# Kernel tuning notes

Measured on AMD Instinct MI355X. Metric: run time of the kernel, lower is better.

## Reference

```python
import jax, jax.numpy as jnp
import numpy as np

B, T = 512, 256
DX, DZ, DH, DDZ, DDX = 1024, 256, 512, 256, 256


def setup_inputs() -> dict:
    key = jax.random.key(0)
    ks = jax.random.split(key, 16)
    s = 0.05
    return {
        "eps": jax.random.normal(ks[0], (B, T, DZ), jnp.float32),
        # stoch_trans dz: h -> relu -> (loc, softplus scale)
        "dz_W1": jax.random.normal(ks[1], (DDZ, DH), jnp.float32) * s,
        "dz_b1": jnp.zeros((DDZ,), jnp.float32),
        "dz_Wloc": jax.random.normal(ks[2], (DZ, DDZ), jnp.float32) * s,
        "dz_bloc": jnp.zeros((DZ,), jnp.float32),
        "dz_Wscale": jax.random.normal(ks[3], (DZ, DDZ), jnp.float32) * s,
        "dz_bscale": jnp.zeros((DZ,), jnp.float32),
        # GRU cell (PyTorch layout: gates [r, z, n] stacked)
        "gru_Wih": jax.random.normal(ks[4], (3 * DH, DZ), jnp.float32) * s,
        "gru_Whh": jax.random.normal(ks[5], (3 * DH, DH), jnp.float32) * s,
        "gru_bih": jnp.zeros((3 * DH,), jnp.float32),
        "gru_bhh": jnp.zeros((3 * DH,), jnp.float32),
        # emitter dx: h -> relu -> sigmoid probs
        "dx_W1": jax.random.normal(ks[6], (DDX, DH), jnp.float32) * s,
        "dx_b1": jnp.zeros((DDX,), jnp.float32),
        "dx_W2": jax.random.normal(ks[7], (DX, DDX), jnp.float32) * s,
        "dx_b2": jnp.zeros((DX,), jnp.float32),
        "h0": jnp.zeros((DH,), jnp.float32),
    }


def reference(eps, dz_W1, dz_b1, dz_Wloc, dz_bloc, dz_Wscale, dz_bscale,
              gru_Wih, gru_Whh, gru_bih, gru_bhh,
              dx_W1, dx_b1, dx_W2, dx_b2, h0):
    batch = eps.shape[0]
    h_init = jnp.broadcast_to(h0[None, :], (batch, h0.shape[0]))

    def step(h, eps_t):
        # stochastic transition: z_loc, z_scale from h_{t-1}
        hid = jax.nn.relu(h @ dz_W1.T + dz_b1)
        z_loc = hid @ dz_Wloc.T + dz_bloc
        z_scale = jax.nn.softplus(hid @ dz_Wscale.T + dz_bscale)
        z_t = z_loc + z_scale * eps_t  # reparameterized Normal sample
        # GRU cell (torch equations)
        gi = z_t @ gru_Wih.T + gru_bih
        gh = h @ gru_Whh.T + gru_bhh
        i_r, i_z, i_n = jnp.split(gi, 3, axis=-1)
        h_r, h_z, h_n = jnp.split(gh, 3, axis=-1)
        r = jax.nn.sigmoid(i_r + h_r)
        u = jax.nn.sigmoid(i_z + h_z)
        n = jnp.tanh(i_n + r * h_n)
        h_new = (1.0 - u) * n + u * h
        # emitter: Bernoulli probs
        hid2 = jax.nn.relu(h_new @ dx_W1.T + dx_b1)
        x_ps = jax.nn.sigmoid(hid2 @ dx_W2.T + dx_b2)
        return h_new, x_ps

    eps_tb = jnp.swapaxes(eps, 0, 1)  # [T, B, DZ]
    _, x_ps = jax.lax.scan(step, h_init, eps_tb)
    return jnp.swapaxes(x_ps, 0, 1)  # [B, T, DX]
```

## Files before the change

kernel.cpp:

```cpp
#include <hip/hip_runtime.h>
#include <hip/hip_bf16.h>

#define DEV __device__ __forceinline__

typedef __bf16 bf16x8 __attribute__((ext_vector_type(8)));
typedef float  f32x4  __attribute__((ext_vector_type(4)));

constexpr int BB  = 512;
constexpr int TT  = 256;
constexpr int DX  = 1024;
constexpr int DZ  = 256;
constexpr int DH  = 512;

DEV f32x4 mfma16(bf16x8 a, bf16x8 b, f32x4 c) {
    return __builtin_amdgcn_mfma_f32_16x16x32_bf16(a, b, c, 0, 0, 0);
}
DEV float sigf(float x) { return 1.0f / (1.0f + __expf(-x)); }
DEV float tanhf_(float x) {
    float e = __expf(-2.0f * fabsf(x));
    float r = (1.0f - e) / (1.0f + e);
    return copysignf(r, x);
}
DEV float softplusf(float x) {
    float m = fmaxf(x, 0.0f);
    return m + __logf(__expf(x - m) + __expf(-m));
}

DEV void st16_wt(void* p, bf16x8 v) {
    asm volatile("global_store_dwordx4 %0, %1, off sc0 sc1" :: "v"(p), "v"(v) : "memory");
}
DEV void st_flag(unsigned* p, unsigned v) {
    asm volatile("global_store_dword %0, %1, off sc0 sc1" :: "v"(p), "v"(v) : "memory");
}
DEV unsigned ld_flag(const unsigned* p) {
    unsigned v;
    asm volatile("global_load_dword %0, %1, off sc0 sc1\n\ts_waitcnt vmcnt(0)"
                 : "=v"(v) : "v"(p) : "memory");
    return v;
}
#define CC_LOAD(dst, p) \
    asm volatile("global_load_dwordx4 %0, %1, off sc0 sc1" : "=v"(dst) : "v"(p))
#define VMCNT0 do { \
    asm volatile("s_waitcnt vmcnt(0)" ::: "memory"); \
    __builtin_amdgcn_sched_barrier(0); } while (0)
#define LGKM0 do { \
    asm volatile("s_waitcnt lgkmcnt(0)" ::: "memory"); \
    __builtin_amdgcn_sched_barrier(0); } while (0)

DEV void wave_wait(const unsigned* base, int nslots, int wv, unsigned tgt) {
    const int lane = threadIdx.x & 63;
    const unsigned* p = base + (((lane & (nslots - 1)) * 4 + wv) * 32);
    while (true) {
        unsigned v = ld_flag(p);
        if (__all((int)(v >= tgt))) break;
    }
}

struct CvtArgs {
    const float* src[7];
    __bf16* dst[7];
    int n[7];
};
__global__ void cvt_weights(CvtArgs a, const float* h0, __bf16* h0buf) {
    int idx = blockIdx.x * blockDim.x + threadIdx.x;
    int stride = gridDim.x * blockDim.x;
    for (int s = 0; s < 7; ++s) {
        const float* sp = a.src[s];
        __bf16* dp = a.dst[s];
        int n = a.n[s];
        for (int i = idx; i < n; i += stride) dp[i] = (__bf16)sp[i];
    }
    for (int i = idx; i < 512 * 512; i += stride) h0buf[i] = (__bf16)h0[i & 511];
}

__global__ __launch_bounds__(256, 1) void phase1c(
    const float* __restrict__ eps,
    const float* __restrict__ b1,  const float* __restrict__ bloc,
    const float* __restrict__ bscale, const float* __restrict__ bih,
    const float* __restrict__ bhh,
    const __bf16* __restrict__ wW1,   const __bf16* __restrict__ wWloc,
    const __bf16* __restrict__ wWscale, const __bf16* __restrict__ wWih,
    const __bf16* __restrict__ wWhh,
    const __bf16* __restrict__ h0buf,
    unsigned* __restrict__ flags,
    char* __restrict__ outb)
{
    __shared__ __bf16 lds[75776];

    const int tid  = threadIdx.x;
    const int w    = tid >> 6;
    const int lane = tid & 63;
    const int r16  = lane & 15;
    const int g4   = lane >> 4;
    const int g    = blockIdx.x & 7;
    const int r    = blockIdx.x >> 3;
    unsigned* gfl   = flags + g * 4096;
    unsigned* flagA = gfl;
    unsigned* flagB = gfl + 2048;
    unsigned* flagC = gfl + 3072;
    const int rowW  = g * 64 + w * 16;

    auto stage = [&](const __bf16* src, __bf16* dst, int R, int C) {
        int chunks = R * C / 8;
        for (int ch = tid; ch < chunks; ch += 256) {
            int row = ch / (C / 8), cc = (ch % (C / 8)) * 8;
            bf16x8 v = *(const bf16x8*)(src + (size_t)row * C + cc);
            *(bf16x8*)(dst + ((row * C + cc) ^ ((row & 7) << 3))) = v;
        }
    };

    if (r < 8) {
        stage(wW1     + (size_t)(r * 32) * 512, lds,         32, 512);
        stage(wWloc   + (size_t)(r * 32) * 256, lds + 16384, 32, 256);
        stage(wWscale + (size_t)(r * 32) * 256, lds + 24576, 32, 256);
        __bf16* wb = lds + 32768 + w * 512;
        const int zc0 = r * 32;
        float bb1[2], bbl[2], bbs[2];
        #pragma unroll
        for (int tt = 0; tt < 2; ++tt) {
            int c = zc0 + tt * 16 + r16;
            bb1[tt] = b1[c]; bbl[tt] = bloc[c]; bbs[tt] = bscale[c];
        }
        __syncthreads();

        for (int t = 0; t < TT; ++t) {
            float ev[2][4];
            #pragma unroll
            for (int tt = 0; tt < 2; ++tt)
                #pragma unroll
                for (int i = 0; i < 4; ++i) {
                    int row = rowW + 4 * g4 + i;
                    ev[tt][i] = __builtin_nontemporal_load(
                        eps + ((size_t)row * TT + t) * DZ + zc0 + tt * 16 + r16);
                }
            if (t) wave_wait(flagA, 16, w, t);
            const char* hp = (t == 0)
                ? (const char*)(h0buf + (size_t)(rowW + r16) * 512) + g4 * 16
                : outb + ((size_t)(rowW + r16) * TT + (t - 1)) * 4096 + 2048 + g4 * 16;
            bf16x8 hv[16];
            #pragma unroll
            for (int kk = 0; kk < 16; ++kk) CC_LOAD(hv[kk], hp + kk * 64);
            VMCNT0;
            f32x4 acc0 = {0,0,0,0}, acc1 = {0,0,0,0};
            #pragma unroll
            for (int kk = 0; kk < 16; ++kk) {
                int l0 = r16, l1 = 16 + r16;
                acc0 = mfma16(hv[kk], *(const bf16x8*)(lds + ((l0 * 512 + kk * 32 + g4 * 8) ^ ((l0 & 7) << 3))), acc0);
                acc1 = mfma16(hv[kk], *(const bf16x8*)(lds + ((l1 * 512 + kk * 32 + g4 * 8) ^ ((l1 & 7) << 3))), acc1);
            }
            #pragma unroll
            for (int tt = 0; tt < 2; ++tt) {
                f32x4 ac = tt ? acc1 : acc0;
                #pragma unroll
                for (int i = 0; i < 4; ++i)
                    wb[(4 * g4 + i) * 32 + tt * 16 + r16] = (__bf16)fmaxf(ac[i] + bb1[tt], 0.0f);
            }
            LGKM0;
            {
                int rl = lane >> 2, ch = lane & 3;
                bf16x8 v = *(const bf16x8*)(wb + rl * 32 + ch * 8);
                st16_wt(outb + ((size_t)(rowW + rl) * TT + t) * 4096 + 3072 + (zc0 + ch * 8) * 2, v);
            }
            VMCNT0;
            if (lane == 0) st_flag(flagB + (r * 4 + w) * 32, t + 1);
            wave_wait(flagB, 8, w, t + 1);
            const char* qp = outb + ((size_t)(rowW + r16) * TT + t) * 4096 + 3072 + g4 * 16;
            bf16x8 qv[8];
            #pragma unroll
            for (int kk = 0; kk < 8; ++kk) CC_LOAD(qv[kk], qp + kk * 64);
            VMCNT0;
            f32x4 aL0 = {0,0,0,0}, aL1 = {0,0,0,0}, aS0 = {0,0,0,0}, aS1 = {0,0,0,0};
            #pragma unroll
            for (int kk = 0; kk < 8; ++kk) {
                int l0 = r16, l1 = 16 + r16;
                int s0 = (l0 * 256 + kk * 32 + g4 * 8) ^ ((l0 & 7) << 3);
                int s1 = (l1 * 256 + kk * 32 + g4 * 8) ^ ((l1 & 7) << 3);
                aL0 = mfma16(qv[kk], *(const bf16x8*)(lds + 16384 + s0), aL0);
                aL1 = mfma16(qv[kk], *(const bf16x8*)(lds + 16384 + s1), aL1);
                aS0 = mfma16(qv[kk], *(const bf16x8*)(lds + 24576 + s0), aS0);
                aS1 = mfma16(qv[kk], *(const bf16x8*)(lds + 24576 + s1), aS1);
            }
            #pragma unroll
            for (int tt = 0; tt < 2; ++tt) {
                f32x4 L = tt ? aL1 : aL0, S = tt ? aS1 : aS0;
                #pragma unroll
                for (int i = 0; i < 4; ++i) {
                    float z = (L[i] + bbl[tt]) + softplusf(S[i] + bbs[tt]) * ev[tt][i];
                    wb[(4 * g4 + i) * 32 + tt * 16 + r16] = (__bf16)z;
                }
            }
            LGKM0;
            {
                int rl = lane >> 2, ch = lane & 3;
                bf16x8 v = *(const bf16x8*)(wb + rl * 32 + ch * 8);
                st16_wt(outb + ((size_t)(rowW + rl) * TT + t) * 4096 + 3584 + (zc0 + ch * 8) * 2, v);
            }
            VMCNT0;
            if (lane == 0) st_flag(flagC + (r * 4 + w) * 32, t + 1);
        }
    } else {
        const int c0 = (r - 8) * 32;
        for (int gg = 0; gg < 3; ++gg) {
            stage(wWhh + (size_t)(512 * gg + c0) * 512, lds + gg * 16384, 32, 512);
            stage(wWih + (size_t)(512 * gg + c0) * 256, lds + 49152 + gg * 8192, 32, 256);
        }
        __bf16* wb = lds + 73728 + w * 512;
        float bI[3][2], bH[3][2];
        #pragma unroll
        for (int gg = 0; gg < 3; ++gg)
            #pragma unroll
            for (int tt = 0; tt < 2; ++tt) {
                int col = 512 * gg + c0 + tt * 16 + r16;
                bI[gg][tt] = bih[col];
                bH[gg][tt] = bhh[col];
            }
        float hreg[2][4];
        #pragma unroll
        for (int tt = 0; tt < 2; ++tt) {
            float v = (float)h0buf[c0 + tt * 16 + r16];
            #pragma unroll
            for (int i = 0; i < 4; ++i) hreg[tt][i] = v;
        }
        __syncthreads();

        for (int t = 0; t < TT; ++t) {
            if (t) wave_wait(flagA, 16, w, t);
            const char* hp = (t == 0)
                ? (const char*)(h0buf + (size_t)(rowW + r16) * 512) + g4 * 16
                : outb + ((size_t)(rowW + r16) * TT + (t - 1)) * 4096 + 2048 + g4 * 16;
            bf16x8 hv[16];
            #pragma unroll
            for (int kk = 0; kk < 16; ++kk) CC_LOAD(hv[kk], hp + kk * 64);
            VMCNT0;
            f32x4 gh[6];
            #pragma unroll
            for (int j = 0; j < 6; ++j) gh[j] = (f32x4){0,0,0,0};
            #pragma unroll
            for (int kk = 0; kk < 16; ++kk) {
                #pragma unroll
                for (int j = 0; j < 6; ++j) {
                    int gg = j >> 1, lr = (j & 1) * 16 + r16;
                    gh[j] = mfma16(hv[kk], *(const bf16x8*)(lds + gg * 16384 +
                              ((lr * 512 + kk * 32 + g4 * 8) ^ ((lr & 7) << 3))), gh[j]);
                }
            }
            wave_wait(flagC, 8, w, t + 1);
            const char* zp = outb + ((size_t)(rowW + r16) * TT + t) * 4096 + 3584 + g4 * 16;
            bf16x8 zv[8];
            #pragma unroll
            for (int kk = 0; kk < 8; ++kk) CC_LOAD(zv[kk], zp + kk * 64);
            VMCNT0;
            f32x4 gi[6];
            #pragma unroll
            for (int j = 0; j < 6; ++j) gi[j] = (f32x4){0,0,0,0};
            #pragma unroll
            for (int kk = 0; kk < 8; ++kk) {
                #pragma unroll
                for (int j = 0; j < 6; ++j) {
                    int gg = j >> 1, lr = (j & 1) * 16 + r16;
                    gi[j] = mfma16(zv[kk], *(const bf16x8*)(lds + 49152 + gg * 8192 +
                              ((lr * 256 + kk * 32 + g4 * 8) ^ ((lr & 7) << 3))), gi[j]);
                }
            }
            #pragma unroll
            for (int tt = 0; tt < 2; ++tt) {
                #pragma unroll
                for (int i = 0; i < 4; ++i) {
                    float rr = sigf(gi[0 + tt][i] + bI[0][tt] + gh[0 + tt][i] + bH[0][tt]);
                    float uu = sigf(gi[2 + tt][i] + bI[1][tt] + gh[2 + tt][i] + bH[1][tt]);
                    float nn = tanhf_(gi[4 + tt][i] + bI[2][tt] + rr * (gh[4 + tt][i] + bH[2][tt]));
                    float hv2 = (1.0f - uu) * nn + uu * hreg[tt][i];
                    hreg[tt][i] = hv2;
                    wb[(4 * g4 + i) * 32 + tt * 16 + r16] = (__bf16)hv2;
                }
            }
            LGKM0;
            {
                int rl = lane >> 2, ch = lane & 3;
                bf16x8 v = *(const bf16x8*)(wb + rl * 32 + ch * 8);
                st16_wt(outb + ((size_t)(rowW + rl) * TT + t) * 4096 + 2048 + (c0 + ch * 8) * 2, v);
            }
            VMCNT0;
            if (lane == 0) st_flag(flagA + ((r - 8) * 4 + w) * 32, t + 1);
        }
    }
}

__global__ __launch_bounds__(256, 3) void phase2(
    const float* __restrict__ db1, const float* __restrict__ db2,
    const __bf16* __restrict__ W1, const __bf16* __restrict__ W2,
    float* __restrict__ out)
{
    __shared__ __bf16 hS  [32 * 512];
    __shared__ __bf16 hid2[32 * 256];

    const int tid  = threadIdx.x;
    const int w    = tid >> 6;
    const int lane = tid & 63;
    const int r16  = lane & 15;
    const int g4   = lane >> 4;
    const size_t row0 = (size_t)blockIdx.x * 32;

    #pragma unroll
    for (int it = 0; it < 8; ++it) {
        int chunk = it * 256 + tid;
        int row = chunk >> 6;
        int cc  = (chunk & 63) * 8;
        bf16x8 v = __builtin_nontemporal_load(
            (const bf16x8*)((const char*)out + (row0 + row) * 4096 + 2048 + cc * 2));
        *(bf16x8*)(hS + ((row * 512 + cc) ^ ((row & 7) << 3))) = v;
    }
    __syncthreads();

    {
        f32x4 acc[2][4];
        #pragma unroll
        for (int rt = 0; rt < 2; ++rt)
            #pragma unroll
            for (int ct = 0; ct < 4; ++ct) acc[rt][ct] = (f32x4){0,0,0,0};
        const __bf16* pB[4];
        #pragma unroll
        for (int ct = 0; ct < 4; ++ct)
            pB[ct] = W1 + (w * 64 + 16 * ct + r16) * 512 + g4 * 8;
        #pragma unroll
        for (int kk = 0; kk < 16; ++kk) {
            bf16x8 a[2];
            #pragma unroll
            for (int rt = 0; rt < 2; ++rt) {
                int row = rt * 16 + r16;
                a[rt] = *(const bf16x8*)(hS + ((row * 512 + kk * 32 + g4 * 8) ^ ((row & 7) << 3)));
            }
            #pragma unroll
            for (int ct = 0; ct < 4; ++ct) {
                bf16x8 b = *(const bf16x8*)(pB[ct] + kk * 32);
                acc[0][ct] = mfma16(a[0], b, acc[0][ct]);
                acc[1][ct] = mfma16(a[1], b, acc[1][ct]);
            }
        }
        #pragma unroll
        for (int ct = 0; ct < 4; ++ct) {
            int col = w * 64 + 16 * ct + r16;
            float bias = db1[col];
            #pragma unroll
            for (int rt = 0; rt < 2; ++rt)
                #pragma unroll
                for (int i = 0; i < 4; ++i) {
                    int row = rt * 16 + g4 * 4 + i;
                    hid2[(row * 256 + col) ^ ((row & 7) << 3)] =
                        (__bf16)fmaxf(acc[rt][ct][i] + bias, 0.0f);
                }
        }
    }
    __syncthreads();

    #pragma unroll
    for (int c = 0; c < 4; ++c) {
        f32x4 acc[2][4];
        #pragma unroll
        for (int rt = 0; rt < 2; ++rt)
            #pragma unroll
            for (int ct = 0; ct < 4; ++ct) acc[rt][ct] = (f32x4){0,0,0,0};
        const __bf16* pB[4];
        #pragma unroll
        for (int ct = 0; ct < 4; ++ct)
            pB[ct] = W2 + (w * 256 + c * 64 + 16 * ct + r16) * 256 + g4 * 8;
        #pragma unroll
        for (int kk = 0; kk < 8; ++kk) {
            bf16x8 a[2];
            #pragma unroll
            for (int rt = 0; rt < 2; ++rt) {
                int row = rt * 16 + r16;
                a[rt] = *(const bf16x8*)(hid2 + ((row * 256 + kk * 32 + g4 * 8) ^ ((row & 7) << 3)));
            }
            #pragma unroll
            for (int ct = 0; ct < 4; ++ct) {
                bf16x8 b = *(const bf16x8*)(pB[ct] + kk * 32);
                acc[0][ct] = mfma16(a[0], b, acc[0][ct]);
                acc[1][ct] = mfma16(a[1], b, acc[1][ct]);
            }
        }
        #pragma unroll
        for (int ct = 0; ct < 4; ++ct) {
            int col = w * 256 + c * 64 + 16 * ct + r16;
            float bias = db2[col];
            #pragma unroll
            for (int rt = 0; rt < 2; ++rt)
                #pragma unroll
                for (int i = 0; i < 4; ++i) {
                    int row = rt * 16 + g4 * 4 + i;
                    __builtin_nontemporal_store(sigf(acc[rt][ct][i] + bias),
                                                out + (row0 + row) * DX + col);
                }
        }
    }
}

extern "C" void kernel_launch(void* const* d_in, const int* in_sizes, int n_in,
                              void* d_out, int out_size, void* d_ws, size_t ws_size,
                              hipStream_t stream) {
    const float* eps       = (const float*)d_in[0];
    const float* dz_W1     = (const float*)d_in[1];
    const float* dz_b1     = (const float*)d_in[2];
    const float* dz_Wloc   = (const float*)d_in[3];
    const float* dz_bloc   = (const float*)d_in[4];
    const float* dz_Wscale = (const float*)d_in[5];
    const float* dz_bscale = (const float*)d_in[6];
    const float* gru_Wih   = (const float*)d_in[7];
    const float* gru_Whh   = (const float*)d_in[8];
    const float* gru_bih   = (const float*)d_in[9];
    const float* gru_bhh   = (const float*)d_in[10];
    const float* dx_W1     = (const float*)d_in[11];
    const float* dx_b1     = (const float*)d_in[12];
    const float* dx_W2     = (const float*)d_in[13];
    const float* dx_b2     = (const float*)d_in[14];
    const float* h0        = (const float*)d_in[15];
    float* out = (float*)d_out;
    char* ws = (char*)d_ws;

    __bf16* wW1     = (__bf16*)(ws + 0);
    __bf16* wWloc   = (__bf16*)(ws + 262144);
    __bf16* wWscale = (__bf16*)(ws + 393216);
    __bf16* wWih    = (__bf16*)(ws + 524288);
    __bf16* wWhh    = (__bf16*)(ws + 1310720);
    __bf16* wdxW1   = (__bf16*)(ws + 2883584);
    __bf16* wdxW2   = (__bf16*)(ws + 3145728);
    __bf16* h0buf   = (__bf16*)(ws + 3670016);
    unsigned* flags = (unsigned*)(ws + 4194304);

    hipMemsetAsync(flags, 0, 131072, stream);

    CvtArgs ca;
    ca.src[0] = dz_W1;     ca.dst[0] = wW1;     ca.n[0] = 256 * 512;
    ca.src[1] = dz_Wloc;   ca.dst[1] = wWloc;   ca.n[1] = 256 * 256;
    ca.src[2] = dz_Wscale; ca.dst[2] = wWscale; ca.n[2] = 256 * 256;
    ca.src[3] = gru_Wih;   ca.dst[3] = wWih;    ca.n[3] = 1536 * 256;
    ca.src[4] = gru_Whh;   ca.dst[4] = wWhh;    ca.n[4] = 1536 * 512;
    ca.src[5] = dx_W1;     ca.dst[5] = wdxW1;   ca.n[5] = 256 * 512;
    ca.src[6] = dx_W2;     ca.dst[6] = wdxW2;   ca.n[6] = 1024 * 256;

    cvt_weights<<<1024, 256, 0, stream>>>(ca, h0, h0buf);
    phase1c<<<192, 256, 0, stream>>>(eps, dz_b1, dz_bloc, dz_bscale,
                                     gru_bih, gru_bhh,
                                     wW1, wWloc, wWscale, wWih, wWhh,
                                     h0buf, flags, (char*)out);
    phase2<<<(BB * TT) / 32, 256, 0, stream>>>(dx_b1, dx_b2, wdxW1, wdxW2, out);
}
```

Measured before the change: 2.819 ms.

## Halve waves per block in recurrent kernel, each wave handles two row slabs

The persistent recurrent kernel now runs 128 threads per block instead of 256. Each wave processes two 16-row sub-slabs sequentially, and flag slots are re-indexed per (wave, sub-slab). This cuts the number of waves contending for the CU and the number of flag pollers, and lets one wave overlap its sub-slab work with the flag waits of another. The cost is that per-step latency per wave roughly doubles and the critical path through the recurrence becomes more serial.

```diff
diff --git a/kernel.cpp b/kernel.cpp
--- a/kernel.cpp
+++ b/kernel.cpp
@@ -47,9 +47,9 @@
     asm volatile("s_waitcnt lgkmcnt(0)" ::: "memory"); \
     __builtin_amdgcn_sched_barrier(0); } while (0)
 
-DEV void wave_wait(const unsigned* base, int nslots, int wv, unsigned tgt) {
+DEV void waitP(const unsigned* base, int mask, int w, int s, unsigned tgt) {
     const int lane = threadIdx.x & 63;
-    const unsigned* p = base + (((lane & (nslots - 1)) * 4 + wv) * 32);
+    const unsigned* p = base + (((lane & mask) * 2 + w) * 2 + s) * 32;
     while (true) {
         unsigned v = ld_flag(p);
         if (__all((int)(v >= tgt))) break;
@@ -73,7 +73,7 @@
     for (int i = idx; i < 512 * 512; i += stride) h0buf[i] = (__bf16)h0[i & 511];
 }
 
-__global__ __launch_bounds__(256, 1) void phase1c(
+__global__ __launch_bounds__(128, 1) void phase1c(
     const float* __restrict__ eps,
     const float* __restrict__ b1,  const float* __restrict__ bloc,
     const float* __restrict__ bscale, const float* __restrict__ bih,
@@ -98,11 +98,11 @@
     unsigned* flagA = gfl;
     unsigned* flagB = gfl + 2048;
     unsigned* flagC = gfl + 3072;
-    const int rowW  = g * 64 + w * 16;
+    const int rowBase = g * 64 + w * 32;
 
     auto stage = [&](const __bf16* src, __bf16* dst, int R, int C) {
         int chunks = R * C / 8;
-        for (int ch = tid; ch < chunks; ch += 256) {
+        for (int ch = tid; ch < chunks; ch += 128) {
             int row = ch / (C / 8), cc = (ch % (C / 8)) * 8;
             bf16x8 v = *(const bf16x8*)(src + (size_t)row * C + cc);
             *(bf16x8*)(dst + ((row * C + cc) ^ ((row & 7) << 3))) = v;
@@ -124,79 +124,89 @@
         __syncthreads();
 
         for (int t = 0; t < TT; ++t) {
-            float ev[2][4];
-            #pragma unroll
-            for (int tt = 0; tt < 2; ++tt)
-                #pragma unroll
-                for (int i = 0; i < 4; ++i) {
-                    int row = rowW + 4 * g4 + i;
-                    ev[tt][i] = __builtin_nontemporal_load(
-                        eps + ((size_t)row * TT + t) * DZ + zc0 + tt * 16 + r16);
-                }
-            if (t) wave_wait(flagA, 16, w, t);
-            const char* hp = (t == 0)
-                ? (const char*)(h0buf + (size_t)(rowW + r16) * 512) + g4 * 16
-                : outb + ((size_t)(rowW + r16) * TT + (t - 1)) * 4096 + 2048 + g4 * 16;
-            bf16x8 hv[16];
-            #pragma unroll
-            for (int kk = 0; kk < 16; ++kk) CC_LOAD(hv[kk], hp + kk * 64);
-            VMCNT0;
-            f32x4 acc0 = {0,0,0,0}, acc1 = {0,0,0,0};
-            #pragma unroll
-            for (int kk = 0; kk < 16; ++kk) {
-                int l0 = r16, l1 = 16 + r16;
-                acc0 = mfma16(hv[kk], *(const bf16x8*)(lds + ((l0 * 512 + kk * 32 + g4 * 8) ^ ((l0 & 7) << 3))), acc0);
-                acc1 = mfma16(hv[kk], *(const bf16x8*)(lds + ((l1 * 512 + kk * 32 + g4 * 8) ^ ((l1 & 7) << 3))), acc1);
-            }
-            #pragma unroll
-            for (int tt = 0; tt < 2; ++tt) {
-                f32x4 ac = tt ? acc1 : acc0;
-                #pragma unroll
-                for (int i = 0; i < 4; ++i)
-                    wb[(4 * g4 + i) * 32 + tt * 16 + r16] = (__bf16)fmaxf(ac[i] + bb1[tt], 0.0f);
-            }
-            LGKM0;
-            {
-                int rl = lane >> 2, ch = lane & 3;
-                bf16x8 v = *(const bf16x8*)(wb + rl * 32 + ch * 8);
-                st16_wt(outb + ((size_t)(rowW + rl) * TT + t) * 4096 + 3072 + (zc0 + ch * 8) * 2, v);
-            }
-            VMCNT0;
-            if (lane == 0) st_flag(flagB + (r * 4 + w) * 32, t + 1);
-            wave_wait(flagB, 8, w, t + 1);
-            const char* qp = outb + ((size_t)(rowW + r16) * TT + t) * 4096 + 3072 + g4 * 16;
-            bf16x8 qv[8];
-            #pragma unroll
-            for (int kk = 0; kk < 8; ++kk) CC_LOAD(qv[kk], qp + kk * 64);
-            VMCNT0;
-            f32x4 aL0 = {0,0,0,0}, aL1 = {0,0,0,0}, aS0 = {0,0,0,0}, aS1 = {0,0,0,0};
-            #pragma unroll
-            for (int kk = 0; kk < 8; ++kk) {
-                int l0 = r16, l1 = 16 + r16;
-                int s0 = (l0 * 256 + kk * 32 + g4 * 8) ^ ((l0 & 7) << 3);
-                int s1 = (l1 * 256 + kk * 32 + g4 * 8) ^ ((l1 & 7) << 3);
-                aL0 = mfma16(qv[kk], *(const bf16x8*)(lds + 16384 + s0), aL0);
-                aL1 = mfma16(qv[kk], *(const bf16x8*)(lds + 16384 + s1), aL1);
-                aS0 = mfma16(qv[kk], *(const bf16x8*)(lds + 24576 + s0), aS0);
-                aS1 = mfma16(qv[kk], *(const bf16x8*)(lds + 24576 + s1), aS1);
-            }
-            #pragma unroll
-            for (int tt = 0; tt < 2; ++tt) {
-                f32x4 L = tt ? aL1 : aL0, S = tt ? aS1 : aS0;
-                #pragma unroll
-                for (int i = 0; i < 4; ++i) {
-                    float z = (L[i] + bbl[tt]) + softplusf(S[i] + bbs[tt]) * ev[tt][i];
-                    wb[(4 * g4 + i) * 32 + tt * 16 + r16] = (__bf16)z;
-                }
-            }
-            LGKM0;
-            {
-                int rl = lane >> 2, ch = lane & 3;
-                bf16x8 v = *(const bf16x8*)(wb + rl * 32 + ch * 8);
-                st16_wt(outb + ((size_t)(rowW + rl) * TT + t) * 4096 + 3584 + (zc0 + ch * 8) * 2, v);
-            }
-            VMCNT0;
-            if (lane == 0) st_flag(flagC + (r * 4 + w) * 32, t + 1);
+            float ev[2][2][4];
+            #pragma unroll
+            for (int s = 0; s < 2; ++s)
+                #pragma unroll
+                for (int tt = 0; tt < 2; ++tt)
+                    #pragma unroll
+                    for (int i = 0; i < 4; ++i) {
+                        int row = rowBase + s * 16 + 4 * g4 + i;
+                        ev[s][tt][i] = __builtin_nontemporal_load(
+                            eps + ((size_t)row * TT + t) * DZ + zc0 + tt * 16 + r16);
+                    }
+            #pragma unroll
+            for (int s = 0; s < 2; ++s) {
+                const int rowS = rowBase + s * 16;
+                if (t) waitP(flagA, 15, w, s, t);
+                const char* hp = (t == 0)
+                    ? (const char*)(h0buf + (size_t)(rowS + r16) * 512) + g4 * 16
+                    : outb + ((size_t)(rowS + r16) * TT + (t - 1)) * 4096 + 2048 + g4 * 16;
+                bf16x8 hv[16];
+                #pragma unroll
+                for (int kk = 0; kk < 16; ++kk) CC_LOAD(hv[kk], hp + kk * 64);
+                VMCNT0;
+                f32x4 acc0 = {0,0,0,0}, acc1 = {0,0,0,0};
+                #pragma unroll
+                for (int kk = 0; kk < 16; ++kk) {
+                    int l0 = r16, l1 = 16 + r16;
+                    acc0 = mfma16(hv[kk], *(const bf16x8*)(lds + ((l0 * 512 + kk * 32 + g4 * 8) ^ ((l0 & 7) << 3))), acc0);
+                    acc1 = mfma16(hv[kk], *(const bf16x8*)(lds + ((l1 * 512 + kk * 32 + g4 * 8) ^ ((l1 & 7) << 3))), acc1);
+                }
+                #pragma unroll
+                for (int tt = 0; tt < 2; ++tt) {
+                    f32x4 ac = tt ? acc1 : acc0;
+                    #pragma unroll
+                    for (int i = 0; i < 4; ++i)
+                        wb[(4 * g4 + i) * 32 + tt * 16 + r16] = (__bf16)fmaxf(ac[i] + bb1[tt], 0.0f);
+                }
+                LGKM0;
+                {
+                    int rl = lane >> 2, ch = lane & 3;
+                    bf16x8 v = *(const bf16x8*)(wb + rl * 32 + ch * 8);
+                    st16_wt(outb + ((size_t)(rowS + rl) * TT + t) * 4096 + 3072 + (zc0 + ch * 8) * 2, v);
+                }
+                VMCNT0;
+                if (lane == 0) st_flag(flagB + ((r * 2 + w) * 2 + s) * 32, t + 1);
+            }
+            #pragma unroll
+            for (int s = 0; s < 2; ++s) {
+                const int rowS = rowBase + s * 16;
+                waitP(flagB, 7, w, s, t + 1);
+                const char* qp = outb + ((size_t)(rowS + r16) * TT + t) * 4096 + 3072 + g4 * 16;
+                bf16x8 qv[8];
+                #pragma unroll
+                for (int kk = 0; kk < 8; ++kk) CC_LOAD(qv[kk], qp + kk * 64);
+                VMCNT0;
+                f32x4 aL0 = {0,0,0,0}, aL1 = {0,0,0,0}, aS0 = {0,0,0,0}, aS1 = {0,0,0,0};
+                #pragma unroll
+                for (int kk = 0; kk < 8; ++kk) {
+                    int l0 = r16, l1 = 16 + r16;
+                    int s0i = (l0 * 256 + kk * 32 + g4 * 8) ^ ((l0 & 7) << 3);
+                    int s1i = (l1 * 256 + kk * 32 + g4 * 8) ^ ((l1 & 7) << 3);
+                    aL0 = mfma16(qv[kk], *(const bf16x8*)(lds + 16384 + s0i), aL0);
+                    aL1 = mfma16(qv[kk], *(const bf16x8*)(lds + 16384 + s1i), aL1);
+                    aS0 = mfma16(qv[kk], *(const bf16x8*)(lds + 24576 + s0i), aS0);
+                    aS1 = mfma16(qv[kk], *(const bf16x8*)(lds + 24576 + s1i), aS1);
+                }
+                #pragma unroll
+                for (int tt = 0; tt < 2; ++tt) {
+                    f32x4 L = tt ? aL1 : aL0, S = tt ? aS1 : aS0;
+                    #pragma unroll
+                    for (int i = 0; i < 4; ++i) {
+                        float z = (L[i] + bbl[tt]) + softplusf(S[i] + bbs[tt]) * ev[s][tt][i];
+                        wb[(4 * g4 + i) * 32 + tt * 16 + r16] = (__bf16)z;
+                    }
+                }
+                LGKM0;
+                {
+                    int rl = lane >> 2, ch = lane & 3;
+                    bf16x8 v = *(const bf16x8*)(wb + rl * 32 + ch * 8);
+                    st16_wt(outb + ((size_t)(rowS + rl) * TT + t) * 4096 + 3584 + (zc0 + ch * 8) * 2, v);
+                }
+                VMCNT0;
+                if (lane == 0) st_flag(flagC + ((r * 2 + w) * 2 + s) * 32, t + 1);
+            }
         }
     } else {
         const int c0 = (r - 8) * 32;
@@ -214,74 +224,84 @@
                 bI[gg][tt] = bih[col];
                 bH[gg][tt] = bhh[col];
             }
-        float hreg[2][4];
+        float hreg[2][2][4];
         #pragma unroll
         for (int tt = 0; tt < 2; ++tt) {
             float v = (float)h0buf[c0 + tt * 16 + r16];
             #pragma unroll
-            for (int i = 0; i < 4; ++i) hreg[tt][i] = v;
+            for (int s = 0; s < 2; ++s)
+                #pragma unroll
+                for (int i = 0; i < 4; ++i) hreg[s][tt][i] = v;
         }
         __syncthreads();
 
         for (int t = 0; t < TT; ++t) {
-            if (t) wave_wait(flagA, 16, w, t);
-            const char* hp = (t == 0)
-                ? (const char*)(h0buf + (size_t)(rowW + r16) * 512) + g4 * 16
-                : outb + ((size_t)(rowW + r16) * TT + (t - 1)) * 4096 + 2048 + g4 * 16;
-            bf16x8 hv[16];
-            #pragma unroll
-            for (int kk = 0; kk < 16; ++kk) CC_LOAD(hv[kk], hp + kk * 64);
-            VMCNT0;
-            f32x4 gh[6];
-            #pragma unroll
-            for (int j = 0; j < 6; ++j) gh[j] = (f32x4){0,0,0,0};
-            #pragma unroll
-            for (int kk = 0; kk < 16; ++kk) {
-                #pragma unroll
-                for (int j = 0; j < 6; ++j) {
-                    int gg = j >> 1, lr = (j & 1) * 16 + r16;
-                    gh[j] = mfma16(hv[kk], *(const bf16x8*)(lds + gg * 16384 +
-                              ((lr * 512 + kk * 32 + g4 * 8) ^ ((lr & 7) << 3))), gh[j]);
-                }
-            }
-            wave_wait(flagC, 8, w, t + 1);
-            const char* zp = outb + ((size_t)(rowW + r16) * TT + t) * 4096 + 3584 + g4 * 16;
-            bf16x8 zv[8];
-            #pragma unroll
-            for (int kk = 0; kk < 8; ++kk) CC_LOAD(zv[kk], zp + kk * 64);
-            VMCNT0;
-            f32x4 gi[6];
-            #pragma unroll
-            for (int j = 0; j < 6; ++j) gi[j] = (f32x4){0,0,0,0};
-            #pragma unroll
-            for (int kk = 0; kk < 8; ++kk) {
-                #pragma unroll
-                for (int j = 0; j < 6; ++j) {
-                    int gg = j >> 1, lr = (j & 1) * 16 + r16;
-                    gi[j] = mfma16(zv[kk], *(const bf16x8*)(lds + 49152 + gg * 8192 +
-                              ((lr * 256 + kk * 32 + g4 * 8) ^ ((lr & 7) << 3))), gi[j]);
-                }
-            }
-            #pragma unroll
-            for (int tt = 0; tt < 2; ++tt) {
-                #pragma unroll
-                for (int i = 0; i < 4; ++i) {
-                    float rr = sigf(gi[0 + tt][i] + bI[0][tt] + gh[0 + tt][i] + bH[0][tt]);
-                    float uu = sigf(gi[2 + tt][i] + bI[1][tt] + gh[2 + tt][i] + bH[1][tt]);
-                    float nn = tanhf_(gi[4 + tt][i] + bI[2][tt] + rr * (gh[4 + tt][i] + bH[2][tt]));
-                    float hv2 = (1.0f - uu) * nn + uu * hreg[tt][i];
-                    hreg[tt][i] = hv2;
-                    wb[(4 * g4 + i) * 32 + tt * 16 + r16] = (__bf16)hv2;
-                }
-            }
-            LGKM0;
-            {
-                int rl = lane >> 2, ch = lane & 3;
-                bf16x8 v = *(const bf16x8*)(wb + rl * 32 + ch * 8);
-                st16_wt(outb + ((size_t)(rowW + rl) * TT + t) * 4096 + 2048 + (c0 + ch * 8) * 2, v);
-            }
-            VMCNT0;
-            if (lane == 0) st_flag(flagA + ((r - 8) * 4 + w) * 32, t + 1);
+            f32x4 gh[2][6];
+            #pragma unroll
+            for (int s = 0; s < 2; ++s) {
+                const int rowS = rowBase + s * 16;
+                if (t) waitP(flagA, 15, w, s, t);
+                const char* hp = (t == 0)
+                    ? (const char*)(h0buf + (size_t)(rowS + r16) * 512) + g4 * 16
+                    : outb + ((size_t)(rowS + r16) * TT + (t - 1)) * 4096 + 2048 + g4 * 16;
+                bf16x8 hv[16];
+                #pragma unroll
+                for (int kk = 0; kk < 16; ++kk) CC_LOAD(hv[kk], hp + kk * 64);
+                VMCNT0;
+                #pragma unroll
+                for (int j = 0; j < 6; ++j) gh[s][j] = (f32x4){0,0,0,0};
+                #pragma unroll
+                for (int kk = 0; kk < 16; ++kk) {
+                    #pragma unroll
+                    for (int j = 0; j < 6; ++j) {
+                        int gg = j >> 1, lr = (j & 1) * 16 + r16;
+                        gh[s][j] = mfma16(hv[kk], *(const bf16x8*)(lds + gg * 16384 +
+                                  ((lr * 512 + kk * 32 + g4 * 8) ^ ((lr & 7) << 3))), gh[s][j]);
+                    }
+                }
+            }
+            #pragma unroll
+            for (int s = 0; s < 2; ++s) {
+                const int rowS = rowBase + s * 16;
+                waitP(flagC, 7, w, s, t + 1);
+                const char* zp = outb + ((size_t)(rowS + r16) * TT + t) * 4096 + 3584 + g4 * 16;
+                bf16x8 zv[8];
+                #pragma unroll
+                for (int kk = 0; kk < 8; ++kk) CC_LOAD(zv[kk], zp + kk * 64);
+                VMCNT0;
+                f32x4 gi[6];
+                #pragma unroll
+                for (int j = 0; j < 6; ++j) gi[j] = (f32x4){0,0,0,0};
+                #pragma unroll
+                for (int kk = 0; kk < 8; ++kk) {
+                    #pragma unroll
+                    for (int j = 0; j < 6; ++j) {
+                        int gg = j >> 1, lr = (j & 1) * 16 + r16;
+                        gi[j] = mfma16(zv[kk], *(const bf16x8*)(lds + 49152 + gg * 8192 +
+                                  ((lr * 256 + kk * 32 + g4 * 8) ^ ((lr & 7) << 3))), gi[j]);
+                    }
+                }
+                #pragma unroll
+                for (int tt = 0; tt < 2; ++tt) {
+                    #pragma unroll
+                    for (int i = 0; i < 4; ++i) {
+                        float rr = sigf(gi[0 + tt][i] + bI[0][tt] + gh[s][0 + tt][i] + bH[0][tt]);
+                        float uu = sigf(gi[2 + tt][i] + bI[1][tt] + gh[s][2 + tt][i] + bH[1][tt]);
+                        float nn = tanhf_(gi[4 + tt][i] + bI[2][tt] + rr * (gh[s][4 + tt][i] + bH[2][tt]));
+                        float hv2 = (1.0f - uu) * nn + uu * hreg[s][tt][i];
+                        hreg[s][tt][i] = hv2;
+                        wb[(4 * g4 + i) * 32 + tt * 16 + r16] = (__bf16)hv2;
+                    }
+                }
+                LGKM0;
+                {
+                    int rl = lane >> 2, ch = lane & 3;
+                    bf16x8 v = *(const bf16x8*)(wb + rl * 32 + ch * 8);
+                    st16_wt(outb + ((size_t)(rowS + rl) * TT + t) * 4096 + 2048 + (c0 + ch * 8) * 2, v);
+                }
+                VMCNT0;
+                if (lane == 0) st_flag(flagA + (((r - 8) * 2 + w) * 2 + s) * 32, t + 1);
+            }
         }
     }
 }
@@ -439,7 +459,7 @@
     ca.src[6] = dx_W2;     ca.dst[6] = wdxW2;   ca.n[6] = 1024 * 256;
 
     cvt_weights<<<1024, 256, 0, stream>>>(ca, h0, h0buf);
-    phase1c<<<192, 256, 0, stream>>>(eps, dz_b1, dz_bloc, dz_bscale,
+    phase1c<<<192, 128, 0, stream>>>(eps, dz_b1, dz_bloc, dz_bscale,
                                      gru_bih, gru_bhh,
                                      wW1, wWloc, wWscale, wWih, wWhh,
                                      h0buf, flags, (char*)out);
```

Measured after the change: 3.762 ms. 1.33x slower.

## Use non-coherent loads/stores when a group's blocks share one XCD; skip self-waits

Applied to the files above, without the earlier changes.

Each block reads its XCC_ID register and publishes it to a roster. Each group of 24 blocks then agrees whether all its members sit on the same XCD. If they do, activation exchanges through global memory use plain loads and stores instead of system-coherent sc0 sc1 accesses, and wave_wait skips polling the block's own flag slot. This aims to cut cross-die cache-bypass latency in the serial recurrence, at the cost of an extra roster handshake. Correctness depends on cache behaviour within one XCD and on whether near stays true, which the scheduler decides.

```diff
diff --git a/kernel.cpp b/kernel.cpp
--- a/kernel.cpp
+++ b/kernel.cpp
@@ -26,9 +26,6 @@
     return m + __logf(__expf(x - m) + __expf(-m));
 }
 
-DEV void st16_wt(void* p, bf16x8 v) {
-    asm volatile("global_store_dwordx4 %0, %1, off sc0 sc1" :: "v"(p), "v"(v) : "memory");
-}
 DEV void st_flag(unsigned* p, unsigned v) {
     asm volatile("global_store_dword %0, %1, off sc0 sc1" :: "v"(p), "v"(v) : "memory");
 }
@@ -38,8 +35,10 @@
                  : "=v"(v) : "v"(p) : "memory");
     return v;
 }
-#define CC_LOAD(dst, p) \
-    asm volatile("global_load_dwordx4 %0, %1, off sc0 sc1" : "=v"(dst) : "v"(p))
+DEV void stx16(void* p, bf16x8 v, bool near) {
+    if (near) asm volatile("global_store_dwordx4 %0, %1, off"         :: "v"(p), "v"(v) : "memory");
+    else      asm volatile("global_store_dwordx4 %0, %1, off sc0 sc1" :: "v"(p), "v"(v) : "memory");
+}
 #define VMCNT0 do { \
     asm volatile("s_waitcnt vmcnt(0)" ::: "memory"); \
     __builtin_amdgcn_sched_barrier(0); } while (0)
@@ -47,12 +46,28 @@
     asm volatile("s_waitcnt lgkmcnt(0)" ::: "memory"); \
     __builtin_amdgcn_sched_barrier(0); } while (0)
 
-DEV void wave_wait(const unsigned* base, int nslots, int wv, unsigned tgt) {
+template <int N>
+DEV void loadN(bf16x8* v, const char* p, bool near) {
+    if (near) {
+        #pragma unroll
+        for (int k = 0; k < N; ++k)
+            asm volatile("global_load_dwordx4 %0, %1, off" : "=v"(v[k]) : "v"(p + k * 64));
+    } else {
+        #pragma unroll
+        for (int k = 0; k < N; ++k)
+            asm volatile("global_load_dwordx4 %0, %1, off sc0 sc1" : "=v"(v[k]) : "v"(p + k * 64));
+    }
+    VMCNT0;
+}
+
+DEV void wave_wait(const unsigned* f, int n, int w, unsigned tgt, int self) {
     const int lane = threadIdx.x & 63;
-    const unsigned* p = base + (((lane & (nslots - 1)) * 4 + wv) * 32);
+    const int slot = lane & (n - 1);
+    const unsigned* p = f + ((slot * 4 + w) * 32);
+    const bool skip = (slot == self);
     while (true) {
         unsigned v = ld_flag(p);
-        if (__all((int)(v >= tgt))) break;
+        if (__all((int)(skip || v >= tgt))) break;
     }
 }
 
@@ -86,6 +101,7 @@
     char* __restrict__ outb)
 {
     __shared__ __bf16 lds[75776];
+    __shared__ int nearFlag;
 
     const int tid  = threadIdx.x;
     const int w    = tid >> 6;
@@ -94,11 +110,17 @@
     const int g4   = lane >> 4;
     const int g    = blockIdx.x & 7;
     const int r    = blockIdx.x >> 3;
-    unsigned* gfl   = flags + g * 4096;
-    unsigned* flagA = gfl;
-    unsigned* flagB = gfl + 2048;
-    unsigned* flagC = gfl + 3072;
+    unsigned* gfl    = flags + g * 4096;
+    unsigned* flagA  = gfl;
+    unsigned* flagB  = gfl + 2048;
+    unsigned* flagC  = gfl + 3072;
+    unsigned* roster = flags + 32768;
     const int rowW  = g * 64 + w * 16;
+
+    unsigned myxcd;
+    asm volatile("s_getreg_b32 %0, hwreg(HW_REG_XCC_ID)" : "=s"(myxcd));
+    myxcd &= 0xf;
+    if (tid == 0) st_flag(roster + (g * 24 + r) * 32, myxcd + 1);
 
     auto stage = [&](const __bf16* src, __bf16* dst, int R, int C) {
         int chunks = R * C / 8;
@@ -106,6 +128,20 @@
             int row = ch / (C / 8), cc = (ch % (C / 8)) * 8;
             bf16x8 v = *(const bf16x8*)(src + (size_t)row * C + cc);
             *(bf16x8*)(dst + ((row * C + cc) ^ ((row & 7) << 3))) = v;
+        }
+    };
+    auto consensus = [&]() {
+        if (tid < 64) {
+            int idx = lane < 24 ? lane : 23;
+            const unsigned* p = roster + (g * 24 + idx) * 32;
+            unsigned v;
+            while (true) {
+                v = ld_flag(p);
+                if (__all((int)(v != 0))) break;
+            }
+            unsigned first = __builtin_amdgcn_readfirstlane(v);
+            int uni = __all((int)(v == first));
+            if (lane == 0) nearFlag = uni;
         }
     };
 
@@ -121,7 +157,9 @@
             int c = zc0 + tt * 16 + r16;
             bb1[tt] = b1[c]; bbl[tt] = bloc[c]; bbs[tt] = bscale[c];
         }
+        consensus();
         __syncthreads();
+        const bool near = nearFlag != 0;
 
         for (int t = 0; t < TT; ++t) {
             float ev[2][4];
@@ -133,14 +171,12 @@
                     ev[tt][i] = __builtin_nontemporal_load(
                         eps + ((size_t)row * TT + t) * DZ + zc0 + tt * 16 + r16);
                 }
-            if (t) wave_wait(flagA, 16, w, t);
+            if (t) wave_wait(flagA, 16, w, t, -1);
             const char* hp = (t == 0)
                 ? (const char*)(h0buf + (size_t)(rowW + r16) * 512) + g4 * 16
                 : outb + ((size_t)(rowW + r16) * TT + (t - 1)) * 4096 + 2048 + g4 * 16;
             bf16x8 hv[16];
-            #pragma unroll
-            for (int kk = 0; kk < 16; ++kk) CC_LOAD(hv[kk], hp + kk * 64);
-            VMCNT0;
+            loadN<16>(hv, hp, near);
             f32x4 acc0 = {0,0,0,0}, acc1 = {0,0,0,0};
             #pragma unroll
             for (int kk = 0; kk < 16; ++kk) {
@@ -159,16 +195,14 @@
             {
                 int rl = lane >> 2, ch = lane & 3;
                 bf16x8 v = *(const bf16x8*)(wb + rl * 32 + ch * 8);
-                st16_wt(outb + ((size_t)(rowW + rl) * TT + t) * 4096 + 3072 + (zc0 + ch * 8) * 2, v);
+                stx16(outb + ((size_t)(rowW + rl) * TT + t) * 4096 + 3072 + (zc0 + ch * 8) * 2, v, near);
             }
             VMCNT0;
             if (lane == 0) st_flag(flagB + (r * 4 + w) * 32, t + 1);
-            wave_wait(flagB, 8, w, t + 1);
+            wave_wait(flagB, 8, w, t + 1, r);
             const char* qp = outb + ((size_t)(rowW + r16) * TT + t) * 4096 + 3072 + g4 * 16;
             bf16x8 qv[8];
-            #pragma unroll
-            for (int kk = 0; kk < 8; ++kk) CC_LOAD(qv[kk], qp + kk * 64);
-            VMCNT0;
+            loadN<8>(qv, qp, near);
             f32x4 aL0 = {0,0,0,0}, aL1 = {0,0,0,0}, aS0 = {0,0,0,0}, aS1 = {0,0,0,0};
             #pragma unroll
             for (int kk = 0; kk < 8; ++kk) {
@@ -193,7 +227,7 @@
             {
                 int rl = lane >> 2, ch = lane & 3;
                 bf16x8 v = *(const bf16x8*)(wb + rl * 32 + ch * 8);
-                st16_wt(outb + ((size_t)(rowW + rl) * TT + t) * 4096 + 3584 + (zc0 + ch * 8) * 2, v);
+                stx16(outb + ((size_t)(rowW + rl) * TT + t) * 4096 + 3584 + (zc0 + ch * 8) * 2, v, near);
             }
             VMCNT0;
             if (lane == 0) st_flag(flagC + (r * 4 + w) * 32, t + 1);
@@ -221,17 +255,17 @@
             #pragma unroll
             for (int i = 0; i < 4; ++i) hreg[tt][i] = v;
         }
+        consensus();
         __syncthreads();
+        const bool near = nearFlag != 0;
 
         for (int t = 0; t < TT; ++t) {
-            if (t) wave_wait(flagA, 16, w, t);
+            if (t) wave_wait(flagA, 16, w, t, r - 8);
             const char* hp = (t == 0)
                 ? (const char*)(h0buf + (size_t)(rowW + r16) * 512) + g4 * 16
                 : outb + ((size_t)(rowW + r16) * TT + (t - 1)) * 4096 + 2048 + g4 * 16;
             bf16x8 hv[16];
-            #pragma unroll
-            for (int kk = 0; kk < 16; ++kk) CC_LOAD(hv[kk], hp + kk * 64);
-            VMCNT0;
+            loadN<16>(hv, hp, near);
             f32x4 gh[6];
             #pragma unroll
             for (int j = 0; j < 6; ++j) gh[j] = (f32x4){0,0,0,0};
@@ -244,12 +278,10 @@
                               ((lr * 512 + kk * 32 + g4 * 8) ^ ((lr & 7) << 3))), gh[j]);
                 }
             }
-            wave_wait(flagC, 8, w, t + 1);
+            wave_wait(flagC, 8, w, t + 1, -1);
             const char* zp = outb + ((size_t)(rowW + r16) * TT + t) * 4096 + 3584 + g4 * 16;
             bf16x8 zv[8];
-            #pragma unroll
-            for (int kk = 0; kk < 8; ++kk) CC_LOAD(zv[kk], zp + kk * 64);
-            VMCNT0;
+            loadN<8>(zv, zp, near);
             f32x4 gi[6];
             #pragma unroll
             for (int j = 0; j < 6; ++j) gi[j] = (f32x4){0,0,0,0};
@@ -278,7 +310,7 @@
             {
                 int rl = lane >> 2, ch = lane & 3;
                 bf16x8 v = *(const bf16x8*)(wb + rl * 32 + ch * 8);
-                st16_wt(outb + ((size_t)(rowW + rl) * TT + t) * 4096 + 2048 + (c0 + ch * 8) * 2, v);
+                stx16(outb + ((size_t)(rowW + rl) * TT + t) * 4096 + 2048 + (c0 + ch * 8) * 2, v, near);
             }
             VMCNT0;
             if (lane == 0) st_flag(flagA + ((r - 8) * 4 + w) * 32, t + 1);
@@ -427,7 +459,7 @@
     __bf16* h0buf   = (__bf16*)(ws + 3670016);
     unsigned* flags = (unsigned*)(ws + 4194304);
 
-    hipMemsetAsync(flags, 0, 131072, stream);
+    hipMemsetAsync(flags, 0, 131072 + 24576, stream);
 
     CvtArgs ca;
     ca.src[0] = dz_W1;     ca.dst[0] = wW1;     ca.n[0] = 256 * 512;
```

New measurement: 2.829 ms. No clear change (+0.4%).
